# Kernel tuning notes

Measured on AMD Instinct MI355X. Metric: run time of the kernel, lower is better.

Reference implementation:

```python
import jax, jax.numpy as jnp
import numpy as np

EPS_SUM = 1e-8
EPS_FILL = 1e-4
NORM_THRESH = 0.1
MASK_THRESH = 0.1


def _shift1(x):
    # conv2d with 1x3 filter [1,1,0], padding (0,1): out[i] = x[i-1] + x[i]
    return x + jnp.pad(x, ((0, 0), (0, 0), (0, 0), (1, 0)))[..., :-1]


def _shift2(x):
    # conv2d with 1x3 filter [0,1,1], padding (0,1): out[i] = x[i] + x[i+1]
    return x + jnp.pad(x, ((0, 0), (0, 0), (0, 0), (0, 1)))[..., 1:]


def _fill(disp, vm, shift_fn, n_steps):
    # Hole filling: each step propagates valid disparity one pixel; after W
    # steps the data-dependent while-loop of the original has converged
    # (further steps are identity), so a fixed-length scan is equivalent.
    def step(carry, _):
        d, m = carry
        m1 = shift_fn(m)
        nm = (m1 > 0).astype(d.dtype)
        d = d * m + shift_fn(d) / (m1 + EPS_FILL) * (nm - m)
        return (d, nm), None
    (disp, vm), _ = jax.lax.scan(step, (disp, vm), None, length=n_steps)
    return disp, vm


def regress_disp(att, valid_mask):
    # att: [B,H,W,W], valid_mask: [B,1,H,W]
    b, h, w, _ = att.shape
    idx = jnp.arange(w, dtype=att.dtype)
    disp_ini = idx[None, None, None, :] - jnp.sum(att * idx, axis=-1).reshape(b, 1, h, w)
    disp = disp_ini * valid_mask
    disp, vm = _fill(disp, valid_mask, _shift1, w)  # left-to-right pass
    disp, vm = _fill(disp, vm, _shift2, w)          # right-to-left pass
    return disp_ini * valid_mask + disp * (1.0 - valid_mask)


def masked_exp_norm(cost, lower):
    # tril/triu-masked exp normalization (non-standard attention)
    tri = jnp.tril if lower else jnp.triu
    c = tri(cost)
    c = jnp.exp(c - jnp.max(c, axis=-1, keepdims=True))
    c = tri(c)
    return c / (jnp.sum(c, axis=-1, keepdims=True) + EPS_SUM)


def gen_pos_shift(w, dtype):
    p = jnp.linspace(0.0, 2.0, w).astype(dtype)
    pos = jnp.maximum(p[:, None] - p[None, :], 0.0)  # pos_l - pos_r, clipped
    return pos[None, None]  # [1,1,W,W]


def gen_raw_disp(att, pos_shift):
    hi = jnp.argmax(att, axis=-1)
    rr = jnp.stack([hi - 1, hi, hi + 1], axis=-1) + 1  # indices into padded axis
    att_pad = jnp.pad(att, ((0, 0), (0, 0), (0, 0), (1, 1)))
    aw = jnp.take_along_axis(att_pad, rr, axis=-1)
    norm = jnp.sum(aw, axis=-1, keepdims=True)
    norm = jnp.where(norm < NORM_THRESH, 1.0, norm)
    aw = aw / norm
    pos_pad = jnp.broadcast_to(jnp.pad(pos_shift, ((0, 0), (0, 0), (0, 0), (1, 1))), att_pad.shape)
    pr = jnp.take_along_axis(pos_pad, rr, axis=-1)
    return jnp.sum(aw * pr, axis=-1)  # [B,H,W]


def setup_inputs() -> dict:
    key = jax.random.key(0)
    k1, k2 = jax.random.split(key)
    B, H, W = 1, 64, 512
    cost1 = jax.random.normal(k1, (B, H, W, W), dtype=jnp.float32)
    cost2 = jax.random.normal(k2, (B, H, W, W), dtype=jnp.float32)
    return {"cost1": cost1, "cost2": cost2}


def reference(cost1, cost2):
    b, h, w, _ = cost1.shape
    att_r2l = masked_exp_norm(cost2, lower=True)   # right-to-left attention
    att_l2r = masked_exp_norm(cost1, lower=False)  # left-to-right attention
    vm_left = (jnp.sum(att_l2r, axis=-2) > MASK_THRESH).astype(cost1.dtype).reshape(b, 1, h, w)
    vm_right = (jnp.sum(att_r2l, axis=-2) > MASK_THRESH).astype(cost1.dtype).reshape(b, 1, h, w)
    disp_r2l = regress_disp(att_r2l, vm_left)   # [B,1,H,W]
    disp_l2r = regress_disp(att_l2r, vm_right)  # [B,1,H,W]
    pos = gen_pos_shift(w, cost1.dtype)
    raw_l2r = gen_raw_disp(att_r2l, pos)                               # [B,H,W]
    raw_r2l = gen_raw_disp(att_l2r, jnp.swapaxes(pos, -1, -2))         # [B,H,W]
    return jnp.concatenate([disp_r2l, disp_l2r, raw_l2r[:, None], raw_r2l[:, None]], axis=1)
```

## Files before the change

### kernel.cpp

```cpp
#include <hip/hip_runtime.h>
#include <float.h>

#define H 64
#define W 512
#define SPLIT 8

__global__ __launch_bounds__(512) void attn_stats_all(
    const float* __restrict__ cost1, const float* __restrict__ cost2,
    float* __restrict__ disp_r2l, float* __restrict__ disp_l2r,
    float* __restrict__ cs_r2l,  float* __restrict__ cs_l2r,
    float* __restrict__ out)
{
  __shared__ float scol[W];
  const int tid  = threadIdx.x;
  const int lane = tid & 63;
  const int wid  = tid >> 6;
  const int gid  = blockIdx.x;
  const bool lower = (gid & 1) == 0;
  const int rest = gid >> 1;
  const int h    = rest / SPLIT;
  const int s    = rest % SPLIT;

  const float* cost = lower ? cost2 : cost1;
  float* disp = lower ? disp_r2l : disp_l2r;
  float* csum = lower ? cs_r2l  : cs_l2r;
  float* raw  = out + (lower ? 2 : 3) * (H * W);

  scol[tid] = 0.f;
  __syncthreads();

  float cacc[8] = {0,0,0,0,0,0,0,0};
  const float pscale = 2.0f / 511.0f;
  const float* hb = cost + (size_t)h * W * W;

  int jmap[8];
  #pragma unroll
  for (int k = 0; k < 8; k++)
    jmap[k] = (k < 4) ? (lane * 4 + k) : (256 + lane * 4 + (k - 4));

  for (int t = wid; t < W / SPLIT; t += 8) {
    const int i = s * (W / SPLIT) + t;
    const float* rp = hb + (size_t)i * W;
    const float4 va = ((const float4*)rp)[lane];
    const float4 vb = ((const float4*)rp)[64 + lane];
    float c[8] = {va.x, va.y, va.z, va.w, vb.x, vb.y, vb.z, vb.w};

    bool vld[8];
    float mxv = -FLT_MAX;
    int   bj  = W;
    #pragma unroll
    for (int k = 0; k < 8; k++) {
      vld[k] = lower ? (jmap[k] <= i) : (jmap[k] >= i);
      if (vld[k] && c[k] > mxv) { mxv = c[k]; bj = jmap[k]; }
    }
    #pragma unroll
    for (int off = 32; off; off >>= 1) {
      const float ov = __shfl_xor(mxv, off);
      const int   oj = __shfl_xor(bj, off);
      if (ov > mxv || (ov == mxv && oj < bj)) { mxv = ov; bj = oj; }
    }
    const int hi = bj;
    float mx = mxv;
    if (lower ? (i < W - 1) : (i > 0)) mx = fmaxf(mx, 0.f);

    float e[8];
    float ssum = 0.f, wsum = 0.f, s0 = 0.f, s1 = 0.f;
    #pragma unroll
    for (int k = 0; k < 8; k++) {
      e[k] = vld[k] ? __expf(c[k] - mx) : 0.f;
      ssum += e[k];
      wsum += e[k] * (float)jmap[k];
      if (jmap[k] >= hi - 1 && jmap[k] <= hi + 1) {
        const float pr = fmaxf((float)(lower ? (i - jmap[k]) : (jmap[k] - i)) * pscale, 0.f);
        s0 += e[k];
        s1 += e[k] * pr;
      }
    }
    #pragma unroll
    for (int off = 32; off; off >>= 1) {
      ssum += __shfl_xor(ssum, off);
      wsum += __shfl_xor(wsum, off);
    }
    const float inv = 1.0f / (ssum + 1e-8f);

    const int jlo = hi > 0 ? hi - 1 : 0;
    const int jh2 = hi < W - 1 ? hi + 1 : W - 1;
    const int l1 = (jlo & 255) >> 2;
    const int l2 = (jh2 & 255) >> 2;
    float t0 = __shfl(s0, l1), t1 = __shfl(s1, l1);
    if (l2 != l1) { t0 += __shfl(s0, l2); t1 += __shfl(s1, l2); }

    #pragma unroll
    for (int k = 0; k < 8; k++) cacc[k] += e[k] * inv;

    if (lane == 0) {
      disp[h * W + i] = (float)i - wsum * inv;
      const float n0 = t0 * inv;
      raw[h * W + i]  = (t1 * inv) / (n0 < 0.1f ? 1.0f : n0);
    }
  }

  #pragma unroll
  for (int k = 0; k < 8; k++) atomicAdd(&scol[jmap[k]], cacc[k]);
  __syncthreads();
  atomicAdd(&csum[h * W + tid], scol[tid]);
}

__global__ __launch_bounds__(64) void fill_rows(
    const float* __restrict__ dispA, const float* __restrict__ csA,
    const float* __restrict__ dispB, const float* __restrict__ csB,
    float* __restrict__ out)
{
  __shared__ float xrow[W];
  const int pair = blockIdx.x >> 6;
  const int h    = blockIdx.x & 63;
  const float* dsp = (pair ? dispB : dispA) + h * W;
  const float* cs  = (pair ? csB  : csA ) + h * W;
  float* o = out + pair * (H * W) + h * W;
  const int lane = threadIdx.x;
  const int j0 = lane * 8;

  float x[8];
  bool m[8];
  int incl[8];
  int run = -1, fv = W;
  #pragma unroll
  for (int k = 0; k < 8; k++) {
    x[k] = dsp[j0 + k];
    m[k] = cs[j0 + k] > 0.1f;
    xrow[j0 + k] = x[k];
    if (m[k]) { run = j0 + k; if (fv == W) fv = j0 + k; }
    incl[k] = run;
  }
  int v = run;
  #pragma unroll
  for (int off = 1; off < 64; off <<= 1) {
    const int tv = __shfl_up(v, off);
    if (lane >= off) v = max(v, tv);
  }
  int excl = __shfl_up(v, 1);
  if (lane == 0) excl = -1;
  int p0 = fv;
  #pragma unroll
  for (int off = 32; off; off >>= 1) p0 = min(p0, __shfl_xor(p0, off));
  __syncthreads();

  const float C2 = -1.4426229e-4f;
  #pragma unroll
  for (int k = 0; k < 8; k++) {
    const int jj = j0 + k;
    float ov;
    if (m[k]) {
      ov = x[k];
    } else {
      const int p = max(excl, incl[k]);
      if (p >= 0)        ov = xrow[p]  * exp2f(C2 * (float)(jj - p));
      else if (p0 < W)   ov = xrow[p0] * exp2f(C2 * (float)(p0 - jj));
      else               ov = 0.f;
    }
    o[jj] = ov;
  }
}

extern "C" void kernel_launch(void* const* d_in, const int* in_sizes, int n_in,
                              void* d_out, int out_size, void* d_ws, size_t ws_size,
                              hipStream_t stream) {
  const float* cost1 = (const float*)d_in[0];
  const float* cost2 = (const float*)d_in[1];
  float* out = (float*)d_out;
  float* w = (float*)d_ws;
  float* disp_r2l_ini = w;
  float* disp_l2r_ini = w + 32768;
  float* cs_l2r       = w + 65536;
  float* cs_r2l       = w + 98304;

  hipMemsetAsync(cs_l2r, 0, 2 * (size_t)H * W * sizeof(float), stream);

  attn_stats_all<<<2 * H * SPLIT, 512, 0, stream>>>(
      cost1, cost2, disp_r2l_ini, disp_l2r_ini, cs_r2l, cs_l2r, out);

  fill_rows<<<2 * H, 64, 0, stream>>>(disp_r2l_ini, cs_l2r,
                                      disp_l2r_ini, cs_r2l, out);
}
```

Baseline: 170.8 us.

## Skip loading fully masked half-rows via templated triangle-aware row processing

```diff
diff --git a/kernel.cpp b/kernel.cpp
--- a/kernel.cpp
+++ b/kernel.cpp
@@ -4,6 +4,112 @@
 #define H 64
 #define W 512
 #define SPLIT 8
+
+template<bool LOWER, bool FULLROW>
+__device__ __forceinline__ void process_rows(
+    const float* __restrict__ hb, const int h, const int s,
+    const int lane, const int wid,
+    float* __restrict__ disp, float* __restrict__ raw, float* scol)
+{
+  constexpr int NH = FULLROW ? 2 : 1;
+  constexpr int JB = FULLROW ? 0 : (LOWER ? 0 : 256);
+  const float pscale = 2.0f / 511.0f;
+
+  float cacc[NH * 4];
+  #pragma unroll
+  for (int q = 0; q < NH * 4; q++) cacc[q] = 0.f;
+
+  int   jmap[NH * 4];
+  float jfmap[NH * 4];
+  #pragma unroll
+  for (int hh = 0; hh < NH; hh++)
+    #pragma unroll
+    for (int k = 0; k < 4; k++) {
+      jmap[hh * 4 + k]  = JB + hh * 256 + lane * 4 + k;
+      jfmap[hh * 4 + k] = (float)jmap[hh * 4 + k];
+    }
+
+  for (int t = wid; t < 64; t += 8) {
+    const int i = s * 64 + t;
+    const float fi = (float)i;
+    const float* rp = hb + (size_t)i * W;
+
+    float c[NH * 4];
+    #pragma unroll
+    for (int hh = 0; hh < NH; hh++) {
+      const float4 v = ((const float4*)rp)[(JB >> 2) + hh * 64 + lane];
+      c[hh*4+0] = v.x; c[hh*4+1] = v.y; c[hh*4+2] = v.z; c[hh*4+3] = v.w;
+    }
+
+    float best = -FLT_MAX;
+    int   bj   = 1024;
+    #pragma unroll
+    for (int hh = 0; hh < NH; hh++) {
+      const bool NM = FULLROW ? (LOWER ? (hh == 1) : (hh == 0)) : true;
+      #pragma unroll
+      for (int k = 0; k < 4; k++) {
+        const int q = hh * 4 + k;
+        float v = c[q];
+        if (NM) {
+          const bool vld = LOWER ? (jmap[q] <= i) : (jmap[q] >= i);
+          v = vld ? v : -FLT_MAX;
+          c[q] = v;
+        }
+        if (v > best) { best = v; bj = jmap[q]; }
+      }
+    }
+    #pragma unroll
+    for (int off = 32; off; off >>= 1) {
+      const float ov = __shfl_xor(best, off);
+      const int   oj = __shfl_xor(bj, off);
+      if (ov > best || (ov == best && oj < bj)) { best = ov; bj = oj; }
+    }
+
+    const int bjm = bj - 1, bjp = bj + 1;
+    const int am = min(max(bjm, 0), W - 1);
+    const int ap = min(bjp, W - 1);
+    const float cm_ = rp[am];
+    const float cp_ = rp[ap];
+
+    const bool hasMasked = LOWER ? (i < W - 1) : (i > 0);
+    const float mx = hasMasked ? fmaxf(best, 0.f) : best;
+
+    float ssum = 0.f, wsum = 0.f;
+    #pragma unroll
+    for (int q = 0; q < NH * 4; q++) {
+      const float e = __expf(c[q] - mx);
+      c[q] = e;
+      ssum += e;
+      wsum = fmaf(e, jfmap[q], wsum);
+    }
+    #pragma unroll
+    for (int off = 32; off; off >>= 1) {
+      ssum += __shfl_xor(ssum, off);
+      wsum += __shfl_xor(wsum, off);
+    }
+    const float inv = 1.f / (ssum + 1e-8f);
+
+    #pragma unroll
+    for (int q = 0; q < NH * 4; q++) cacc[q] = fmaf(c[q], inv, cacc[q]);
+
+    if (lane == 0) {
+      const bool pv = LOWER ? (bjm >= 0) : (bjm >= i);
+      const bool nv = LOWER ? (bjp <= i) : (bjp <= W - 1);
+      const float e_h = __expf(best - mx);
+      const float e_p = pv ? __expf(cm_ - mx) : 0.f;
+      const float e_n = nv ? __expf(cp_ - mx) : 0.f;
+      const float t0 = e_p + e_h + e_n;
+      const float w0 = fmaf(e_p, (float)bjm, fmaf(e_h, (float)bj, e_n * (float)bjp));
+      disp[h * W + i] = fi - wsum * inv;
+      const float n0 = t0 * inv;
+      const float t1 = pscale * (LOWER ? (fi * t0 - w0) : (w0 - fi * t0));
+      raw[h * W + i] = (t1 * inv) / (n0 < 0.1f ? 1.f : n0);
+    }
+  }
+
+  #pragma unroll
+  for (int q = 0; q < NH * 4; q++) atomicAdd(&scol[jmap[q]], cacc[q]);
+}
 
 __global__ __launch_bounds__(512) void attn_stats_all(
     const float* __restrict__ cost1, const float* __restrict__ cost2,
@@ -18,92 +124,30 @@
   const int gid  = blockIdx.x;
   const bool lower = (gid & 1) == 0;
   const int rest = gid >> 1;
-  const int h    = rest / SPLIT;
-  const int s    = rest % SPLIT;
+  const int h    = rest >> 3;
+  const int s    = rest & 7;
 
   const float* cost = lower ? cost2 : cost1;
   float* disp = lower ? disp_r2l : disp_l2r;
   float* csum = lower ? cs_r2l  : cs_l2r;
   float* raw  = out + (lower ? 2 : 3) * (H * W);
+  const float* hb = cost + (size_t)h * W * W;
 
   scol[tid] = 0.f;
   __syncthreads();
 
-  float cacc[8] = {0,0,0,0,0,0,0,0};
-  const float pscale = 2.0f / 511.0f;
-  const float* hb = cost + (size_t)h * W * W;
-
-  int jmap[8];
-  #pragma unroll
-  for (int k = 0; k < 8; k++)
-    jmap[k] = (k < 4) ? (lane * 4 + k) : (256 + lane * 4 + (k - 4));
-
-  for (int t = wid; t < W / SPLIT; t += 8) {
-    const int i = s * (W / SPLIT) + t;
-    const float* rp = hb + (size_t)i * W;
-    const float4 va = ((const float4*)rp)[lane];
-    const float4 vb = ((const float4*)rp)[64 + lane];
-    float c[8] = {va.x, va.y, va.z, va.w, vb.x, vb.y, vb.z, vb.w};
-
-    bool vld[8];
-    float mxv = -FLT_MAX;
-    int   bj  = W;
-    #pragma unroll
-    for (int k = 0; k < 8; k++) {
-      vld[k] = lower ? (jmap[k] <= i) : (jmap[k] >= i);
-      if (vld[k] && c[k] > mxv) { mxv = c[k]; bj = jmap[k]; }
-    }
-    #pragma unroll
-    for (int off = 32; off; off >>= 1) {
-      const float ov = __shfl_xor(mxv, off);
-      const int   oj = __shfl_xor(bj, off);
-      if (ov > mxv || (ov == mxv && oj < bj)) { mxv = ov; bj = oj; }
-    }
-    const int hi = bj;
-    float mx = mxv;
-    if (lower ? (i < W - 1) : (i > 0)) mx = fmaxf(mx, 0.f);
-
-    float e[8];
-    float ssum = 0.f, wsum = 0.f, s0 = 0.f, s1 = 0.f;
-    #pragma unroll
-    for (int k = 0; k < 8; k++) {
-      e[k] = vld[k] ? __expf(c[k] - mx) : 0.f;
-      ssum += e[k];
-      wsum += e[k] * (float)jmap[k];
-      if (jmap[k] >= hi - 1 && jmap[k] <= hi + 1) {
-        const float pr = fmaxf((float)(lower ? (i - jmap[k]) : (jmap[k] - i)) * pscale, 0.f);
-        s0 += e[k];
-        s1 += e[k] * pr;
-      }
-    }
-    #pragma unroll
-    for (int off = 32; off; off >>= 1) {
-      ssum += __shfl_xor(ssum, off);
-      wsum += __shfl_xor(wsum, off);
-    }
-    const float inv = 1.0f / (ssum + 1e-8f);
-
-    const int jlo = hi > 0 ? hi - 1 : 0;
-    const int jh2 = hi < W - 1 ? hi + 1 : W - 1;
-    const int l1 = (jlo & 255) >> 2;
-    const int l2 = (jh2 & 255) >> 2;
-    float t0 = __shfl(s0, l1), t1 = __shfl(s1, l1);
-    if (l2 != l1) { t0 += __shfl(s0, l2); t1 += __shfl(s1, l2); }
-
-    #pragma unroll
-    for (int k = 0; k < 8; k++) cacc[k] += e[k] * inv;
-
-    if (lane == 0) {
-      disp[h * W + i] = (float)i - wsum * inv;
-      const float n0 = t0 * inv;
-      raw[h * W + i]  = (t1 * inv) / (n0 < 0.1f ? 1.0f : n0);
-    }
-  }
-
-  #pragma unroll
-  for (int k = 0; k < 8; k++) atomicAdd(&scol[jmap[k]], cacc[k]);
+  if (lower) {
+    if (s < 4) process_rows<true,  false>(hb, h, s, lane, wid, disp, raw, scol);
+    else       process_rows<true,  true >(hb, h, s, lane, wid, disp, raw, scol);
+  } else {
+    if (s < 4) process_rows<false, true >(hb, h, s, lane, wid, disp, raw, scol);
+    else       process_rows<false, false>(hb, h, s, lane, wid, disp, raw, scol);
+  }
   __syncthreads();
-  atomicAdd(&csum[h * W + tid], scol[tid]);
+
+  const bool doMine = lower ? (s >= 4 || tid < 256)
+                            : (s < 4  || tid >= 256);
+  if (doMine) atomicAdd(&csum[h * W + tid], scol[tid]);
 }
 
 __global__ __launch_bounds__(64) void fill_rows(
```

New measurement: 163.1 us. 4.5% less time.
